# Kernel tuning notes

Hardware: AMD Instinct MI355X
Metric: run time of the kernel (lower is better)

Reference implementation:

```python
import jax, jax.numpy as jnp
import numpy as np

B, N, IN_F = 8, 1024, 512
H, D = 4, 128  # num_heads, out_features; H*D == IN_F for residual
LN_EPS = 1e-5
NEG_INF = -1e9


def setup_inputs() -> dict:
    key = jax.random.key(0)
    ks = jax.random.split(key, 7)
    x = jax.random.normal(ks[0], (B, N, IN_F), dtype=jnp.float32)
    mask = jax.random.randint(ks[1], (B, N), 0, 2, dtype=jnp.int32)
    # xavier-uniform-ish init scales
    W = jax.random.uniform(ks[2], (IN_F, H * D), dtype=jnp.float32, minval=-1.0, maxval=1.0) * (1.414 * np.sqrt(6.0 / (IN_F + H * D)))
    a_src = jax.random.uniform(ks[3], (H, D), dtype=jnp.float32, minval=-1.0, maxval=1.0) * (1.414 * np.sqrt(6.0 / (H + D)))
    a_dst = jax.random.uniform(ks[4], (H, D), dtype=jnp.float32, minval=-1.0, maxval=1.0) * (1.414 * np.sqrt(6.0 / (H + D)))
    gamma = jnp.ones((H * D,), dtype=jnp.float32)
    beta = jnp.zeros((H * D,), dtype=jnp.float32)
    return {"x": x, "mask": mask, "W": W, "a_src": a_src, "a_dst": a_dst, "gamma": gamma, "beta": beta}


def _layernorm(y, gamma, beta):
    mu = jnp.mean(y, axis=-1, keepdims=True)
    var = jnp.var(y, axis=-1, keepdims=True)
    return (y - mu) * jax.lax.rsqrt(var + LN_EPS) * gamma + beta


def reference(x, mask, W, a_src, a_dst, gamma, beta):
    b, n, _ = x.shape
    h = (x @ W).reshape(b, n, H, D)                      # [B,N,H,D]
    e_i = jnp.einsum('bnhd,hd->bnh', h, a_src)           # [B,N,H]
    e_j = jnp.einsum('bnhd,hd->bnh', h, a_dst)           # [B,N,H]
    e = jax.nn.leaky_relu(e_i[:, :, None, :] + e_j[:, None, :, :], 0.2)  # [B,N,N,H]
    mm = mask[:, None, :, None] * mask[:, :, None, None]  # [B,N,N,1]
    e = jnp.where(mm == 0, NEG_INF, e)
    attn = jax.nn.softmax(e, axis=2)                     # softmax over neighbors j
    h_prime = jnp.einsum('bnjh,bjhd->bnhd', attn, h).reshape(b, n, H * D)
    return _layernorm(h_prime + x, gamma, beta)
```

## Files before the change

kernel.cpp:

```cpp
#include <hip/hip_runtime.h>
#include <math.h>

#define Bsz 8
#define Nn 1024
#define Ff 512
#define Hh 4
#define Dd 128

typedef float f32x4 __attribute__((ext_vector_type(4)));
typedef short bf16x8 __attribute__((ext_vector_type(8)));

__device__ inline uint f2b1(float a) {
    union { float f; uint u; } v; v.f = a;
    return (v.u + 0x7fffu + ((v.u >> 16) & 1u)) >> 16;
}
__device__ inline uint f2b_pk(float a, float b) { return f2b1(a) | (f2b1(b) << 16); }


__global__ __launch_bounds__(256) void conv_xw(const float* __restrict__ X,
                                               const float* __restrict__ Wm,
                                               ushort* __restrict__ Xc,
                                               ushort* __restrict__ Wc) {
    const int bi = blockIdx.x, tid = threadIdx.x;
    if (bi < 512) {
        const int mtile = bi, kblk = tid >> 2, m15b = (tid & 3) * 4;
        #pragma unroll
        for (int c = 0; c < 4; ++c) {
            int m15 = m15b + c;
            const float4* xp = (const float4*)(X + (size_t)(mtile * 16 + m15) * Ff + kblk * 8);
            float4 f0 = xp[0], f1 = xp[1];
            uint4 o = { f2b_pk(f0.x, f0.y), f2b_pk(f0.z, f0.w),
                        f2b_pk(f1.x, f1.y), f2b_pk(f1.z, f1.w) };
            *(uint4*)(Xc + (((size_t)(mtile * 64 + kblk) * 16 + m15) << 3)) = o;
        }
    } else {
        int id = (bi - 512) * 256 + tid;
        int n15 = id & 15, nt = (id >> 4) & 7, kblk = (id >> 7) & 63, nc = id >> 13;
        int col = nc * 128 + nt * 16 + n15;
        float v[8];
        #pragma unroll
        for (int u = 0; u < 8; ++u)
            v[u] = Wm[(size_t)(kblk * 8 + u) * Ff + col];
        uint4 o = { f2b_pk(v[0], v[1]), f2b_pk(v[2], v[3]),
                    f2b_pk(v[4], v[5]), f2b_pk(v[6], v[7]) };
        *(uint4*)(Wc + ((size_t)id << 3)) = o;
    }
}

__global__ __launch_bounds__(256, 4) void gemm_xw(const ushort* __restrict__ Xc,
                                                  const ushort* __restrict__ Wc,
                                                  const float* __restrict__ a_src,
                                                  const float* __restrict__ a_dst,
                                                  ushort* __restrict__ hT,
                                                  float* __restrict__ ei,
                                                  float* __restrict__ ej) {
    const int idx = blockIdx.x;
    const int b = idx & 7, mi = (idx >> 3) & 15, nq = idx >> 7;
    const int nc = nq >> 1, nh = nq & 1;
    const int tid = threadIdx.x;
    const int w = tid >> 6, lane = tid & 63, quad = lane >> 4, l16 = lane & 15;
    const int mtile = (b * 16 + mi) * 4 + w;

    f32x4 z = {0.f, 0.f, 0.f, 0.f};
    f32x4 acc[4];
    #pragma unroll
    for (int t = 0; t < 4; ++t) acc[t] = z;

    const ushort* ap = Xc + ((size_t)mtile << 13) + quad * 128 + l16 * 8;
    const ushort* bp = Wc + ((size_t)nc << 16) + nh * 512 + quad * 1024 + l16 * 8;

    bf16x8 ac = *(const bf16x8*)(ap);
    bf16x8 bc[4];
    #pragma unroll
    for (int t = 0; t < 4; ++t) bc[t] = *(const bf16x8*)(bp + t * 128);

    #pragma unroll 4
    for (int s = 0; s < 16; ++s) {
        bf16x8 an, bn[4];
        if (s < 15) {
            an = *(const bf16x8*)(ap + (s + 1) * 512);
            #pragma unroll
            for (int t = 0; t < 4; ++t)
                bn[t] = *(const bf16x8*)(bp + (s + 1) * 4096 + t * 128);
        }
        #pragma unroll
        for (int t = 0; t < 4; ++t)
            acc[t] = __builtin_amdgcn_mfma_f32_16x16x32_bf16(ac, bc[t], acc[t], 0, 0, 0);
        if (s < 15) {
            ac = an;
            #pragma unroll
            for (int t = 0; t < 4; ++t) bc[t] = bn[t];
        }
    }

    const int nseq = (mi * 4 + w) * 16 + quad * 4;
    const int jb = nseq >> 5, js = nseq & 31;
    #pragma unroll
    for (int t = 0; t < 4; ++t) {
        uint2 pv;
        pv.x = f2b_pk(acc[t][0], acc[t][1]);
        pv.y = f2b_pk(acc[t][2], acc[t][3]);
        int hd = nc * 128 + (nh * 4 + t) * 16 + l16;
        *(uint2*)(hT + ((size_t)(b * 32 + jb)) * 16384 + (size_t)hd * 32 + js) = pv;
    }

    {
        float as4[4], ad4[4];
        #pragma unroll
        for (int t = 0; t < 4; ++t) {
            int hd = nc * 128 + (nh * 4 + t) * 16 + l16;
            as4[t] = a_src[hd];
            ad4[t] = a_dst[hd];
        }
        #pragma unroll
        for (int rr = 0; rr < 4; ++rr) {
            float v1 = 0.f, v2 = 0.f;
            #pragma unroll
            for (int t = 0; t < 4; ++t) {
                v1 += acc[t][rr] * as4[t];
                v2 += acc[t][rr] * ad4[t];
            }
            #pragma unroll
            for (int off = 1; off < 16; off <<= 1) {
                v1 += __shfl_xor(v1, off);
                v2 += __shfl_xor(v2, off);
            }
            if (l16 == 0) {
                int n = nseq + rr;
                atomicAdd(ei + ((b * 4 + nc) << 10) + n, v1);
                atomicAdd(ej + ((b * 4 + nc) << 10) + n, v2);
            }
        }
    }
}

__global__ __launch_bounds__(512, 2) void attn_pv(const ushort* __restrict__ hT,
                                                  const float* __restrict__ ei_g,
                                                  const float* __restrict__ ej_g,
                                                  const int* __restrict__ mask,
                                                  const float* __restrict__ X,
                                                  const float* __restrict__ gamma,
                                                  const float* __restrict__ beta,
                                                  float* __restrict__ out) {
    __shared__ float s_ep[32 * 516];
    __shared__ float s_as[4][32];

    const int idx = blockIdx.x;
    const int b = idx & 7, i0 = (idx >> 3) * 32;
    const int tid = threadIdx.x;
    const int w = tid >> 6, w4 = w & 3, jh = w >> 2;
    const int lane = tid & 63, quad = lane >> 4, l16 = lane & 15;

    const float* ejh = ej_g + ((b * 4 + w4) << 10);
    const int* mkb = mask + (b << 10);

    float maxej = -3.0e38f;
    #pragma unroll
    for (int k = 0; k < 16; ++k) maxej = fmaxf(maxej, ejh[lane + 64 * k]);
    #pragma unroll
    for (int off = 1; off < 64; off <<= 1) maxej = fmaxf(maxej, __shfl_xor(maxej, off));

    const float ei0 = ei_g[((b * 4 + w4) << 10) + i0 + l16];
    const float ei1 = ei_g[((b * 4 + w4) << 10) + i0 + 16 + l16];
    const int mi0 = mkb[i0 + l16];
    const int mi1 = mkb[i0 + 16 + l16];
    float m0, m1;
    { float t = ei0 + maxej; m0 = mi0 ? fmaxf(t, 0.2f * t) : -1e9f; }
    { float t = ei1 + maxej; m1 = mi1 ? fmaxf(t, 0.2f * t) : -1e9f; }

    f32x4 z = {0.f, 0.f, 0.f, 0.f};
    f32x4 acc[2][8], asum[2];
    #pragma unroll
    for (int it = 0; it < 2; ++it) { asum[it] = z;
        #pragma unroll
        for (int dt = 0; dt < 8; ++dt) acc[it][dt] = z; }
    bf16x8 ones;
    #pragma unroll
    for (int q = 0; q < 8; ++q) ones[q] = (short)0x3F80;

    const ushort* hTb = hT + ((size_t)(b * 32)) * 16384 + (size_t)(w4 * 128) * 32
                        + l16 * 32 + quad * 8;

    bf16x8 cur[8];
    {
        const ushort* h0 = hTb + (size_t)(jh * 16) * 16384;
        #pragma unroll
        for (int dt = 0; dt < 8; ++dt) cur[dt] = *(const bf16x8*)(h0 + dt * 512);
    }

    #pragma unroll 2
    for (int r = 0; r < 16; ++r) {
        bf16x8 nxt[8];
        if (r < 15) {
            const ushort* hn = hTb + (size_t)(jh * 16 + r + 1) * 16384;
            #pragma unroll
            for (int dt = 0; dt < 8; ++dt) nxt[dt] = *(const bf16x8*)(hn + dt * 512);
        }
        const int jq = (jh * 16 + r) * 32 + quad * 8;
        float4 e0 = *(const float4*)(ejh + jq);
        float4 e1 = *(const float4*)(ejh + jq + 4);
        int4 q0 = *(const int4*)(mkb + jq);
        int4 q1 = *(const int4*)(mkb + jq + 4);
        float ev[8] = {e0.x, e0.y, e0.z, e0.w, e1.x, e1.y, e1.z, e1.w};
        int   mv[8] = {q0.x, q0.y, q0.z, q0.w, q1.x, q1.y, q1.z, q1.w};
        float wv0[8], wv1[8];
        #pragma unroll
        for (int u = 0; u < 8; ++u) {
            float t0 = ei0 + ev[u];
            float l0 = fmaxf(t0, 0.2f * t0);
            wv0[u] = __expf(((mi0 && mv[u]) ? l0 : -1e9f) - m0);
            float t1 = ei1 + ev[u];
            float l1 = fmaxf(t1, 0.2f * t1);
            wv1[u] = __expf(((mi1 && mv[u]) ? l1 : -1e9f) - m1);
        }
        union { uint4 u; bf16x8 v; } af0, af1;
        af0.u.x = f2b_pk(wv0[0], wv0[1]); af0.u.y = f2b_pk(wv0[2], wv0[3]);
        af0.u.z = f2b_pk(wv0[4], wv0[5]); af0.u.w = f2b_pk(wv0[6], wv0[7]);
        af1.u.x = f2b_pk(wv1[0], wv1[1]); af1.u.y = f2b_pk(wv1[2], wv1[3]);
        af1.u.z = f2b_pk(wv1[4], wv1[5]); af1.u.w = f2b_pk(wv1[6], wv1[7]);
        asum[0] = __builtin_amdgcn_mfma_f32_16x16x32_bf16(af0.v, ones, asum[0], 0, 0, 0);
        asum[1] = __builtin_amdgcn_mfma_f32_16x16x32_bf16(af1.v, ones, asum[1], 0, 0, 0);
        #pragma unroll
        for (int dt = 0; dt < 8; ++dt) {
            acc[0][dt] = __builtin_amdgcn_mfma_f32_16x16x32_bf16(af0.v, cur[dt], acc[0][dt], 0, 0, 0);
            acc[1][dt] = __builtin_amdgcn_mfma_f32_16x16x32_bf16(af1.v, cur[dt], acc[1][dt], 0, 0, 0);
        }
        if (r < 15) {
            #pragma unroll
            for (int dt = 0; dt < 8; ++dt) cur[dt] = nxt[dt];
        }
    }

    if (jh == 1) {
        #pragma unroll
        for (int it = 0; it < 2; ++it)
            #pragma unroll
            for (int dt = 0; dt < 8; ++dt)
                #pragma unroll
                for (int rr = 0; rr < 4; ++rr)
                    s_ep[(it * 16 + quad * 4 + rr) * 516 + w4 * 128 + dt * 16 + l16] =
                        acc[it][dt][rr];
        if (l16 == 0) {
            #pragma unroll
            for (int it = 0; it < 2; ++it)
                #pragma unroll
                for (int rr = 0; rr < 4; ++rr)
                    s_as[w4][it * 16 + quad * 4 + rr] = asum[it][rr];
        }
    }
    __syncthreads();
    if (jh == 0) {
        float rs[2][4];
        #pragma unroll
        for (int it = 0; it < 2; ++it)
            #pragma unroll
            for (int rr = 0; rr < 4; ++rr)
                rs[it][rr] = 1.f / (asum[it][rr] + s_as[w4][it * 16 + quad * 4 + rr]);
        #pragma unroll
        for (int it = 0; it < 2; ++it)
            #pragma unroll
            for (int dt = 0; dt < 8; ++dt)
                #pragma unroll
                for (int rr = 0; rr < 4; ++rr) {
                    int off = (it * 16 + quad * 4 + rr) * 516 + w4 * 128 + dt * 16 + l16;
                    s_ep[off] = (acc[it][dt][rr] + s_ep[off]) * rs[it][rr];
                }
    }
    __syncthreads();

    #pragma unroll
    for (int q = 0; q < 4; ++q) {
        int ir = w * 4 + q;
        int ig = i0 + ir;
        float4 p0 = *(const float4*)(&s_ep[ir * 516 + lane * 8]);
        float4 p1 = *(const float4*)(&s_ep[ir * 516 + lane * 8 + 4]);
        const float* xp = X + (((size_t)((b << 10) + ig)) << 9) + lane * 8;
        float4 x0 = *(const float4*)(xp);
        float4 x1 = *(const float4*)(xp + 4);
        float v[8] = {p0.x + x0.x, p0.y + x0.y, p0.z + x0.z, p0.w + x0.w,
                      p1.x + x1.x, p1.y + x1.y, p1.z + x1.z, p1.w + x1.w};
        float s1 = 0.f, s2 = 0.f;
        #pragma unroll
        for (int u = 0; u < 8; ++u) { s1 += v[u]; s2 += v[u] * v[u]; }
        #pragma unroll
        for (int off = 1; off < 64; off <<= 1) { s1 += __shfl_xor(s1, off); s2 += __shfl_xor(s2, off); }
        float mean = s1 * (1.f / 512.f);
        float var  = s2 * (1.f / 512.f) - mean * mean;
        float rstd = rsqrtf(var + 1e-5f);
        int f0i = lane * 8;
        float4 g0 = *(const float4*)(gamma + f0i);
        float4 g1 = *(const float4*)(gamma + f0i + 4);
        float4 be0 = *(const float4*)(beta + f0i);
        float4 be1 = *(const float4*)(beta + f0i + 4);
        float* op = out + (((size_t)((b << 10) + ig)) << 9) + f0i;
        float4 o0, o1;
        o0.x = (v[0] - mean) * rstd * g0.x + be0.x;
        o0.y = (v[1] - mean) * rstd * g0.y + be0.y;
        o0.z = (v[2] - mean) * rstd * g0.z + be0.z;
        o0.w = (v[3] - mean) * rstd * g0.w + be0.w;
        o1.x = (v[4] - mean) * rstd * g1.x + be1.x;
        o1.y = (v[5] - mean) * rstd * g1.y + be1.y;
        o1.z = (v[6] - mean) * rstd * g1.z + be1.z;
        o1.w = (v[7] - mean) * rstd * g1.w + be1.w;
        *(float4*)op = o0;
        *(float4*)(op + 4) = o1;
    }
}

extern "C" void kernel_launch(void* const* d_in, const int* in_sizes, int n_in,
                              void* d_out, int out_size, void* d_ws, size_t ws_size,
                              hipStream_t stream) {
    const float* x     = (const float*)d_in[0];
    const int*   mask  = (const int*)d_in[1];
    const float* W     = (const float*)d_in[2];
    const float* a_src = (const float*)d_in[3];
    const float* a_dst = (const float*)d_in[4];
    const float* gamma = (const float*)d_in[5];
    const float* beta  = (const float*)d_in[6];
    float* out = (float*)d_out;

    ushort* hT = (ushort*)d_ws;
    ushort* Xc = hT + (size_t)8 * 512 * 1024;
    ushort* Wc = Xc + (size_t)8 * 1024 * 512;
    float* ei = (float*)(Wc + (size_t)512 * 512);
    float* ej = ei + 32768;

    hipMemsetAsync(ei, 0, 2 * 32768 * sizeof(float), stream);
    conv_xw<<<dim3(640), 256, 0, stream>>>(x, W, Xc, Wc);
    gemm_xw<<<dim3(1024), 256, 0, stream>>>(Xc, Wc, a_src, a_dst, hT, ei, ej);
    attn_pv<<<dim3(256), 512, 0, stream>>>(hT, ei, ej, mask, x, gamma, beta, out);
}
```

Measured before the change: 133.8 us.

## Widen GEMM tile to full head, drop atomics and memset, coalesce W conversion

```diff
diff --git a/kernel.cpp b/kernel.cpp
--- a/kernel.cpp
+++ b/kernel.cpp
@@ -21,6 +21,7 @@
                                                const float* __restrict__ Wm,
                                                ushort* __restrict__ Xc,
                                                ushort* __restrict__ Wc) {
+    __shared__ float tile[8 * 520];
     const int bi = blockIdx.x, tid = threadIdx.x;
     if (bi < 512) {
         const int mtile = bi, kblk = tid >> 2, m15b = (tid & 3) * 4;
@@ -34,16 +35,29 @@
             *(uint4*)(Xc + (((size_t)(mtile * 64 + kblk) * 16 + m15) << 3)) = o;
         }
     } else {
-        int id = (bi - 512) * 256 + tid;
-        int n15 = id & 15, nt = (id >> 4) & 7, kblk = (id >> 7) & 63, nc = id >> 13;
-        int col = nc * 128 + nt * 16 + n15;
-        float v[8];
-        #pragma unroll
-        for (int u = 0; u < 8; ++u)
-            v[u] = Wm[(size_t)(kblk * 8 + u) * Ff + col];
-        uint4 o = { f2b_pk(v[0], v[1]), f2b_pk(v[2], v[3]),
-                    f2b_pk(v[4], v[5]), f2b_pk(v[6], v[7]) };
-        *(uint4*)(Wc + ((size_t)id << 3)) = o;
+        const int kb = bi - 512;
+        const int l = tid & 63, wv = tid >> 6;
+        const int col0 = l * 8;
+        #pragma unroll
+        for (int rsel = 0; rsel < 2; ++rsel) {
+            int kr = wv + rsel * 4;
+            const float4* wp = (const float4*)(Wm + (size_t)(kb * 8 + kr) * Ff + col0);
+            float4 a = wp[0], c = wp[1];
+            *(float4*)(&tile[kr * 520 + col0]) = a;
+            *(float4*)(&tile[kr * 520 + col0 + 4]) = c;
+        }
+        __syncthreads();
+        #pragma unroll
+        for (int rsel = 0; rsel < 2; ++rsel) {
+            int n = tid + rsel * 256;
+            float v[8];
+            #pragma unroll
+            for (int u = 0; u < 8; ++u) v[u] = tile[u * 520 + n];
+            uint4 o = { f2b_pk(v[0], v[1]), f2b_pk(v[2], v[3]),
+                        f2b_pk(v[4], v[5]), f2b_pk(v[6], v[7]) };
+            int nc = n >> 7, nt = (n >> 4) & 7, n15 = n & 15;
+            *(uint4*)(Wc + ((size_t)(((nc * 64 + kb) * 8 + nt) * 16 + n15) << 3)) = o;
+        }
     }
 }
 
@@ -55,70 +69,69 @@
                                                   float* __restrict__ ei,
                                                   float* __restrict__ ej) {
     const int idx = blockIdx.x;
-    const int b = idx & 7, mi = (idx >> 3) & 15, nq = idx >> 7;
-    const int nc = nq >> 1, nh = nq & 1;
+    const int b = idx & 7, sub = idx >> 3;
+    const int mi = sub & 15, nc = sub >> 4;
     const int tid = threadIdx.x;
     const int w = tid >> 6, lane = tid & 63, quad = lane >> 4, l16 = lane & 15;
     const int mtile = (b * 16 + mi) * 4 + w;
 
     f32x4 z = {0.f, 0.f, 0.f, 0.f};
-    f32x4 acc[4];
-    #pragma unroll
-    for (int t = 0; t < 4; ++t) acc[t] = z;
+    f32x4 acc[8];
+    #pragma unroll
+    for (int nt = 0; nt < 8; ++nt) acc[nt] = z;
 
     const ushort* ap = Xc + ((size_t)mtile << 13) + quad * 128 + l16 * 8;
-    const ushort* bp = Wc + ((size_t)nc << 16) + nh * 512 + quad * 1024 + l16 * 8;
+    const ushort* bp = Wc + ((size_t)nc << 16) + quad * 1024 + l16 * 8;
 
     bf16x8 ac = *(const bf16x8*)(ap);
-    bf16x8 bc[4];
-    #pragma unroll
-    for (int t = 0; t < 4; ++t) bc[t] = *(const bf16x8*)(bp + t * 128);
-
-    #pragma unroll 4
+    bf16x8 bc[8];
+    #pragma unroll
+    for (int nt = 0; nt < 8; ++nt) bc[nt] = *(const bf16x8*)(bp + nt * 128);
+
+    #pragma unroll 2
     for (int s = 0; s < 16; ++s) {
-        bf16x8 an, bn[4];
+        bf16x8 an, bn[8];
         if (s < 15) {
             an = *(const bf16x8*)(ap + (s + 1) * 512);
             #pragma unroll
-            for (int t = 0; t < 4; ++t)
-                bn[t] = *(const bf16x8*)(bp + (s + 1) * 4096 + t * 128);
-        }
-        #pragma unroll
-        for (int t = 0; t < 4; ++t)
-            acc[t] = __builtin_amdgcn_mfma_f32_16x16x32_bf16(ac, bc[t], acc[t], 0, 0, 0);
+            for (int nt = 0; nt < 8; ++nt)
+                bn[nt] = *(const bf16x8*)(bp + (s + 1) * 4096 + nt * 128);
+        }
+        #pragma unroll
+        for (int nt = 0; nt < 8; ++nt)
+            acc[nt] = __builtin_amdgcn_mfma_f32_16x16x32_bf16(ac, bc[nt], acc[nt], 0, 0, 0);
         if (s < 15) {
             ac = an;
             #pragma unroll
-            for (int t = 0; t < 4; ++t) bc[t] = bn[t];
+            for (int nt = 0; nt < 8; ++nt) bc[nt] = bn[nt];
         }
     }
 
     const int nseq = (mi * 4 + w) * 16 + quad * 4;
     const int jb = nseq >> 5, js = nseq & 31;
     #pragma unroll
-    for (int t = 0; t < 4; ++t) {
+    for (int nt = 0; nt < 8; ++nt) {
         uint2 pv;
-        pv.x = f2b_pk(acc[t][0], acc[t][1]);
-        pv.y = f2b_pk(acc[t][2], acc[t][3]);
-        int hd = nc * 128 + (nh * 4 + t) * 16 + l16;
+        pv.x = f2b_pk(acc[nt][0], acc[nt][1]);
+        pv.y = f2b_pk(acc[nt][2], acc[nt][3]);
+        int hd = nc * 128 + nt * 16 + l16;
         *(uint2*)(hT + ((size_t)(b * 32 + jb)) * 16384 + (size_t)hd * 32 + js) = pv;
     }
 
     {
-        float as4[4], ad4[4];
-        #pragma unroll
-        for (int t = 0; t < 4; ++t) {
-            int hd = nc * 128 + (nh * 4 + t) * 16 + l16;
-            as4[t] = a_src[hd];
-            ad4[t] = a_dst[hd];
+        float as4[8], ad4[8];
+        #pragma unroll
+        for (int nt = 0; nt < 8; ++nt) {
+            as4[nt] = a_src[nc * 128 + nt * 16 + l16];
+            ad4[nt] = a_dst[nc * 128 + nt * 16 + l16];
         }
         #pragma unroll
         for (int rr = 0; rr < 4; ++rr) {
             float v1 = 0.f, v2 = 0.f;
             #pragma unroll
-            for (int t = 0; t < 4; ++t) {
-                v1 += acc[t][rr] * as4[t];
-                v2 += acc[t][rr] * ad4[t];
+            for (int nt = 0; nt < 8; ++nt) {
+                v1 += acc[nt][rr] * as4[nt];
+                v2 += acc[nt][rr] * ad4[nt];
             }
             #pragma unroll
             for (int off = 1; off < 16; off <<= 1) {
@@ -127,8 +140,8 @@
             }
             if (l16 == 0) {
                 int n = nseq + rr;
-                atomicAdd(ei + ((b * 4 + nc) << 10) + n, v1);
-                atomicAdd(ej + ((b * 4 + nc) << 10) + n, v2);
+                ei[((b * 4 + nc) << 10) + n] = v1;
+                ej[((b * 4 + nc) << 10) + n] = v2;
             }
         }
     }
@@ -325,8 +338,7 @@
     float* ei = (float*)(Wc + (size_t)512 * 512);
     float* ej = ei + 32768;
 
-    hipMemsetAsync(ei, 0, 2 * 32768 * sizeof(float), stream);
-    conv_xw<<<dim3(640), 256, 0, stream>>>(x, W, Xc, Wc);
-    gemm_xw<<<dim3(1024), 256, 0, stream>>>(Xc, Wc, a_src, a_dst, hT, ei, ej);
+    conv_xw<<<dim3(576), 256, 0, stream>>>(x, W, Xc, Wc);
+    gemm_xw<<<dim3(512), 256, 0, stream>>>(Xc, Wc, a_src, a_dst, hT, ei, ej);
     attn_pv<<<dim3(256), 512, 0, stream>>>(hT, ei, ej, mask, x, gamma, beta, out);
 }
```

Measured after the change: 131.9 us. No clear change (-1.4%).
